# Performance work log

Measured on AMD Instinct MI355X. Metric: run time of the kernel, lower is better.

The kernel has to match this reference:

```python
import jax, jax.numpy as jnp
import numpy as np

N_NODES = 100000
N_EDGES = 1600000
D_IN = 128
D_OUT = 128
EPS = 1e-5


def setup_inputs() -> dict:
    key = jax.random.key(0)
    k1, k2, k3, k4, k5 = jax.random.split(key, 5)
    x = jax.random.normal(k1, (N_NODES, D_IN), dtype=jnp.float32)
    row = jax.random.randint(k2, (N_EDGES,), 0, N_NODES, dtype=jnp.int64)
    col = jax.random.randint(k3, (N_EDGES,), 0, N_NODES, dtype=jnp.int64)
    adj_vals = jax.random.uniform(k4, (N_EDGES,), dtype=jnp.float32)
    # Xavier-uniform init for weight, zeros for bias (as in the torch module)
    limit = float(np.sqrt(6.0 / (D_IN + D_OUT)))
    weight = jax.random.uniform(k5, (D_IN, D_OUT), minval=-limit, maxval=limit, dtype=jnp.float32)
    bias = jnp.zeros((D_OUT,), dtype=jnp.float32)
    return {"x": x, "row": row, "col": col, "adj_vals": adj_vals, "weight": weight, "bias": bias}


def reference(x, row, col, adj_vals, weight, bias):
    # degree = row-sum of sparse adj
    degree = jax.ops.segment_sum(adj_vals, row, num_segments=N_NODES)
    degree = jnp.where(degree == 0, EPS, degree)
    d_inv_sqrt = (degree + EPS) ** -0.5  # [N]
    # edge-wise symmetric normalization: D^-1/2 A D^-1/2
    edge_w = d_inv_sqrt[row] * adj_vals * d_inv_sqrt[col]  # [E]
    # SpMM: gather neighbor features, scale, scatter-add to destination rows
    msgs = edge_w[:, None] * x[col]  # [E, D_IN]
    agg = jax.ops.segment_sum(msgs, row, num_segments=N_NODES)  # [N, D_IN]
    return agg @ weight + bias
```

## Files before the change

kernel.cpp:

```cpp
#include <hip/hip_runtime.h>

#define NN 100000
#define NE 1600000
#define D  128
#define EPS 1e-5f

#define NBKT   782
#define NEB    391
#define EPB_H  4096
#define NSCAN  (NBKT*NEB)
#define CAP    2560
#define SLW    16

#define OFF_HCNT 0x0000000ULL
#define OFF_BTOT 0x0140000ULL
#define OFF_DINV 0x0150000ULL
#define OFF_RBC  0x0200000ULL
#define OFF_GREC 0x0280000ULL
#define OFF_ECOL 0x11C6000ULL
#define OFF_YB   0x1A00000ULL

typedef short short8 __attribute__((ext_vector_type(8)));
typedef float f32x4 __attribute__((ext_vector_type(4)));

static __device__ __forceinline__ unsigned f2bf(float f) {
    unsigned u = __float_as_uint(f);
    return (u + 0x7fffu + ((u >> 16) & 1u)) >> 16;
}

__global__ void k0h(const int* __restrict__ row, unsigned* __restrict__ hcnt) {
    __shared__ unsigned h[NBKT];
    int t = threadIdx.x, b = blockIdx.x;
    for (int i = t; i < NBKT; i += 256) h[i] = 0;
    __syncthreads();
    int ebeg = b * EPB_H;
    for (int i = t; i < EPB_H; i += 256) {
        int e = ebeg + i;
        if (e < NE) atomicAdd(&h[((unsigned)row[e]) >> 7], 1u);
    }
    __syncthreads();
    for (int i = t; i < NBKT; i += 256) hcnt[i * NEB + b] = h[i];
}

__global__ void k2s(unsigned* __restrict__ hcnt, unsigned* __restrict__ btot) {
    __shared__ unsigned s[256];
    int t = threadIdx.x, b = blockIdx.x;
    unsigned* hp = hcnt + (size_t)b * NEB;
    unsigned v0 = (2 * t     < NEB) ? hp[2 * t]     : 0;
    unsigned v1 = (2 * t + 1 < NEB) ? hp[2 * t + 1] : 0;
    unsigned sum = v0 + v1;
    s[t] = sum;
    __syncthreads();
    for (int d = 1; d < 256; d <<= 1) {
        unsigned u = (t >= d) ? s[t - d] : 0;
        __syncthreads();
        s[t] += u;
        __syncthreads();
    }
    unsigned base = s[t] - sum;
    if (2 * t     < NEB) hp[2 * t]     = base;
    if (2 * t + 1 < NEB) hp[2 * t + 1] = base + v0;
    if (t == 255) btot[b] = s[255];
}

__launch_bounds__(256)
__global__ void k3(const int* __restrict__ row, const int* __restrict__ col,
                   const float* __restrict__ adj, const unsigned* __restrict__ hcnt,
                   unsigned long long* __restrict__ grec) {
    __shared__ unsigned cur[NBKT];
    int t = threadIdx.x, b = blockIdx.x;
    for (int i = t; i < NBKT; i += 256)
        cur[i] = (unsigned)i * CAP + hcnt[i * NEB + b];
    __syncthreads();
    int ebeg = b * EPB_H;
    for (int i = t; i < EPB_H; i += 256) {
        int e = ebeg + i;
        if (e >= NE) continue;
        unsigned r = (unsigned)row[e];
        unsigned bkt = r >> 7;
        unsigned aq = (unsigned)rintf(adj[e] * 32767.0f);
        unsigned lo = (unsigned)col[e] | (aq << 17);
        unsigned dst = atomicAdd(&cur[bkt], 1u);
        if (dst < (bkt + 1) * (unsigned)CAP)
            grec[dst] = (unsigned long long)lo | ((unsigned long long)(r & 127u) << 32);
    }
}

__launch_bounds__(256, 2)
__global__ void k1g(const float* __restrict__ x, const float* __restrict__ w,
                    const unsigned* __restrict__ btot,
                    const unsigned long long* __restrict__ grec,
                    float* __restrict__ dinv_g, unsigned* __restrict__ rbcnt_g,
                    unsigned* __restrict__ ecol_g, unsigned short* __restrict__ yb) {
    __shared__ unsigned short sx[128 * 128];
    __shared__ unsigned short sw[128 * 128];
    __shared__ unsigned sdeg[128], scnt[128], srb[128], scur[128];
    __shared__ float sdv[128];
    unsigned* secol = (unsigned*)sx;
    int tid = threadIdx.x;
    int b = blockIdx.x;
    int base = b * 128;

    if (tid < 128) { sdeg[tid] = 0; scnt[tid] = 0; }
    __syncthreads();
    unsigned beg = (unsigned)b * CAP;
    unsigned n = min(btot[b], (unsigned)CAP);
    unsigned end = beg + n;
    for (unsigned p = beg + tid; p < end; p += 256) {
        unsigned long long rec = grec[p];
        unsigned rid = (unsigned)(rec >> 32) & 127u;
        atomicAdd(&sdeg[rid], ((unsigned)rec >> 17) & 0x7FFFu);
        atomicAdd(&scnt[rid], 1u);
    }
    __syncthreads();

    if (tid < 128) {
        float d = (float)sdeg[tid] * (1.0f / 32767.0f);
        d = (d == 0.0f) ? EPS : d;
        float dv = rsqrtf(d + EPS);
        sdv[tid] = dv;
        int r = base + tid;
        if (r < NN) dinv_g[r] = dv;
        srb[tid] = scnt[tid];
    }
    __syncthreads();
    for (int dd = 1; dd < 128; dd <<= 1) {
        unsigned u = (tid >= dd && tid < 128) ? srb[tid - dd] : 0;
        __syncthreads();
        if (tid < 128) srb[tid] += u;
        __syncthreads();
    }
    if (tid < 128) {
        unsigned rb = srb[tid] - scnt[tid];
        srb[tid] = rb;
        scur[tid] = rb;
        rbcnt_g[b * 128 + tid] = (rb << 16) | scnt[tid];
    }
    __syncthreads();

    for (unsigned p = beg + tid; p < end; p += 256) {
        unsigned long long rec = grec[p];
        unsigned rank = atomicAdd(&scur[(unsigned)(rec >> 32) & 127u], 1u);
        if (rank < CAP) secol[rank] = (unsigned)rec;
    }
    __syncthreads();
    for (unsigned i = tid; i < n; i += 256) ecol_g[(size_t)b * CAP + i] = secol[i];
    __syncthreads();

    #pragma unroll
    for (int i = 0; i < 8; ++i) {
        int task = i * 256 + tid;
        int nn = task & 127, ko = task >> 7;
        const float* wp = w + (size_t)(ko * 8) * D + nn;
        uint4 pk;
        pk.x = f2bf(wp[0])     | (f2bf(wp[D])     << 16);
        pk.y = f2bf(wp[2 * D]) | (f2bf(wp[3 * D]) << 16);
        pk.z = f2bf(wp[4 * D]) | (f2bf(wp[5 * D]) << 16);
        pk.w = f2bf(wp[6 * D]) | (f2bf(wp[7 * D]) << 16);
        int idx = (nn * 128 + ko * 8) ^ ((nn & 7) << 3);
        *(uint4*)(&sw[idx]) = pk;
    }
    #pragma unroll
    for (int i = 0; i < 8; ++i) {
        int task = i * 256 + tid;
        int ko = task & 15, r = task >> 4;
        int gr = base + r;
        float4 f0 = make_float4(0.f, 0.f, 0.f, 0.f), f1 = f0;
        if (gr < NN) {
            const float* xp = x + (size_t)gr * D + ko * 8;
            f0 = *(const float4*)xp;
            f1 = *(const float4*)(xp + 4);
        }
        uint4 pk;
        pk.x = f2bf(f0.x) | (f2bf(f0.y) << 16);
        pk.y = f2bf(f0.z) | (f2bf(f0.w) << 16);
        pk.z = f2bf(f1.x) | (f2bf(f1.y) << 16);
        pk.w = f2bf(f1.z) | (f2bf(f1.w) << 16);
        int idx = (r * 128 + ko * 8) ^ ((r & 7) << 3);
        *(uint4*)(&sx[idx]) = pk;
    }
    __syncthreads();

    int wv = tid >> 6, l = tid & 63;
    int lr = l & 15, g = l >> 4;

    f32x4 acc[2][8];
    #pragma unroll
    for (int ti = 0; ti < 2; ++ti)
        #pragma unroll
        for (int tj = 0; tj < 8; ++tj)
            acc[ti][tj] = (f32x4){0.f, 0.f, 0.f, 0.f};

    #pragma unroll
    for (int kc = 0; kc < 4; ++kc) {
        int kb = kc * 32 + g * 8;
        short8 a[2], bb[8];
        #pragma unroll
        for (int ti = 0; ti < 2; ++ti) {
            int r0 = wv * 32 + ti * 16 + lr;
            a[ti] = *(const short8*)(&sx[(r0 * 128 + kb) ^ ((r0 & 7) << 3)]);
        }
        #pragma unroll
        for (int tj = 0; tj < 8; ++tj) {
            int n0 = tj * 16 + lr;
            bb[tj] = *(const short8*)(&sw[(n0 * 128 + kb) ^ ((n0 & 7) << 3)]);
        }
        #pragma unroll
        for (int ti = 0; ti < 2; ++ti)
            #pragma unroll
            for (int tj = 0; tj < 8; ++tj)
                acc[ti][tj] = __builtin_amdgcn_mfma_f32_16x16x32_bf16(
                    a[ti], bb[tj], acc[ti][tj], 0, 0, 0);
    }

    #pragma unroll
    for (int ti = 0; ti < 2; ++ti) {
        #pragma unroll
        for (int reg = 0; reg < 4; ++reg) {
            int lrow = wv * 32 + ti * 16 + g * 4 + reg;
            int gr = base + lrow;
            if (gr < NN) {
                float dv = sdv[lrow];
                #pragma unroll
                for (int tj = 0; tj < 8; ++tj)
                    yb[(size_t)tj * ((size_t)NN * SLW) + (size_t)gr * SLW + lr] =
                        (unsigned short)f2bf(acc[ti][tj][reg] * dv);
            }
        }
    }
}

__launch_bounds__(256, 4)
__global__ void k4b(const unsigned* __restrict__ rbcnt_g, const unsigned* __restrict__ ecol_g,
                    const float* __restrict__ dinv, const unsigned short* __restrict__ ybs,
                    const float* __restrict__ bias, float* __restrict__ out) {
    __shared__ unsigned ecol[CAP + 8];
    __shared__ unsigned rb_l[128], cnt_l[128];
    __shared__ unsigned nsh;
    int t = threadIdx.x, bid = blockIdx.x;
    int s = bid & 7;
    int q = bid >> 3;
    const unsigned short* ys = ybs + (size_t)s * ((size_t)NN * SLW);

    if (t < 128) {
        unsigned v = rbcnt_g[q * 128 + t];
        rb_l[t] = v >> 16;
        cnt_l[t] = v & 0xFFFFu;
        if (t == 127) nsh = min((v >> 16) + (v & 0xFFFFu), (unsigned)CAP);
    }
    __syncthreads();
    unsigned n = nsh;
    const unsigned* eg = ecol_g + (size_t)q * CAP;
    for (unsigned i = t; i < n; i += 256) ecol[i] = eg[i];
    __syncthreads();

    int grp = t >> 1, lq = t & 1;
    int r = q * 128 + grp;
    if (r >= NN) return;
    unsigned jb = rb_l[grp];
    unsigned jend = min(jb + cnt_l[grp], (unsigned)CAP);

    float a0 = 0.f, a1 = 0.f, a2 = 0.f, a3 = 0.f;
    float a4 = 0.f, a5 = 0.f, a6 = 0.f, a7 = 0.f;

    for (unsigned j = jb; j < jend; j += 8) {
        unsigned ee[8];
        uint4 yq[8];
        float wv[8];
        int cm[8];
        unsigned c0 = ecol[j] & 0x1FFFFu;
        #pragma unroll
        for (int u = 0; u < 8; ++u) ee[u] = ecol[j + u];
        #pragma unroll
        for (int u = 0; u < 8; ++u)
            cm[u] = (j + u < jend) ? (int)(ee[u] & 0x1FFFFu) : (int)c0;
        #pragma unroll
        for (int u = 0; u < 8; ++u)
            yq[u] = *(const uint4*)(ys + (size_t)cm[u] * SLW + lq * 8);
        #pragma unroll
        for (int u = 0; u < 8; ++u)
            wv[u] = (j + u < jend) ? (float)(ee[u] >> 17) : 0.f;
        #pragma unroll
        for (int u = 0; u < 8; ++u) {
            a0 += wv[u] * __uint_as_float(yq[u].x << 16);
            a1 += wv[u] * __uint_as_float(yq[u].x & 0xffff0000u);
            a2 += wv[u] * __uint_as_float(yq[u].y << 16);
            a3 += wv[u] * __uint_as_float(yq[u].y & 0xffff0000u);
            a4 += wv[u] * __uint_as_float(yq[u].z << 16);
            a5 += wv[u] * __uint_as_float(yq[u].z & 0xffff0000u);
            a6 += wv[u] * __uint_as_float(yq[u].w << 16);
            a7 += wv[u] * __uint_as_float(yq[u].w & 0xffff0000u);
        }
    }

    float scale = dinv[r] * (1.0f / 32767.0f);
    const float4* bp = (const float4*)(bias + s * SLW + lq * 8);
    float4* op = (float4*)(out + (size_t)r * D + s * SLW + lq * 8);
    float4 b0 = bp[0], b1 = bp[1];
    op[0] = make_float4(a0 * scale + b0.x, a1 * scale + b0.y,
                        a2 * scale + b0.z, a3 * scale + b0.w);
    op[1] = make_float4(a4 * scale + b1.x, a5 * scale + b1.y,
                        a6 * scale + b1.z, a7 * scale + b1.w);
}

extern "C" void kernel_launch(void* const* d_in, const int* in_sizes, int n_in,
                              void* d_out, int out_size, void* d_ws, size_t ws_size,
                              hipStream_t stream) {
    const float* x    = (const float*)d_in[0];
    const int*   row  = (const int*)d_in[1];
    const int*   col  = (const int*)d_in[2];
    const float* adj  = (const float*)d_in[3];
    const float* wgt  = (const float*)d_in[4];
    const float* bias = (const float*)d_in[5];
    float* out = (float*)d_out;
    char*  ws  = (char*)d_ws;

    unsigned* hcnt  = (unsigned*)(ws + OFF_HCNT);
    unsigned* btot  = (unsigned*)(ws + OFF_BTOT);
    float*    dinv  = (float*)(ws + OFF_DINV);
    unsigned* rbcnt = (unsigned*)(ws + OFF_RBC);
    unsigned long long* grec = (unsigned long long*)(ws + OFF_GREC);
    unsigned* ecolg = (unsigned*)(ws + OFF_ECOL);
    unsigned short* yb = (unsigned short*)(ws + OFF_YB);

    k0h<<<NEB, 256, 0, stream>>>(row, hcnt);
    k2s<<<NBKT, 256, 0, stream>>>(hcnt, btot);
    k3 <<<NEB, 256, 0, stream>>>(row, col, adj, hcnt, grec);
    k1g<<<NBKT, 256, 0, stream>>>(x, wgt, btot, grec, dinv, rbcnt, ecolg, yb);
    k4b<<<NBKT * 8, 256, 0, stream>>>(rbcnt, ecolg, dinv, yb, bias, out);
}
```

Baseline: 148.1 us.

## Store projected features row-major and split SpMM into two 64-column halves

```diff
diff --git a/kernel.cpp b/kernel.cpp
--- a/kernel.cpp
+++ b/kernel.cpp
@@ -10,7 +10,6 @@
 #define EPB_H  4096
 #define NSCAN  (NBKT*NEB)
 #define CAP    2560
-#define SLW    16
 
 #define OFF_HCNT 0x0000000ULL
 #define OFF_BTOT 0x0140000ULL
@@ -223,24 +222,26 @@
                 float dv = sdv[lrow];
                 #pragma unroll
                 for (int tj = 0; tj < 8; ++tj)
-                    yb[(size_t)tj * ((size_t)NN * SLW) + (size_t)gr * SLW + lr] =
+                    yb[(size_t)gr * D + tj * 16 + lr] =
                         (unsigned short)f2bf(acc[ti][tj][reg] * dv);
             }
         }
     }
 }
 
-__launch_bounds__(256, 4)
+__launch_bounds__(512, 4)
 __global__ void k4b(const unsigned* __restrict__ rbcnt_g, const unsigned* __restrict__ ecol_g,
-                    const float* __restrict__ dinv, const unsigned short* __restrict__ ybs,
+                    const float* __restrict__ dinv, const unsigned short* __restrict__ yb,
                     const float* __restrict__ bias, float* __restrict__ out) {
     __shared__ unsigned ecol[CAP + 8];
     __shared__ unsigned rb_l[128], cnt_l[128];
     __shared__ unsigned nsh;
     int t = threadIdx.x, bid = blockIdx.x;
-    int s = bid & 7;
-    int q = bid >> 3;
-    const unsigned short* ys = ybs + (size_t)s * ((size_t)NN * SLW);
+    int xcd = bid & 7;
+    int ch  = xcd >> 2;
+    int q   = (bid >> 3) * 4 + (xcd & 3);
+    if (q >= NBKT) return;
+    int cb = ch * 64;
 
     if (t < 128) {
         unsigned v = rbcnt_g[q * 128 + t];
@@ -251,56 +252,60 @@
     __syncthreads();
     unsigned n = nsh;
     const unsigned* eg = ecol_g + (size_t)q * CAP;
-    for (unsigned i = t; i < n; i += 256) ecol[i] = eg[i];
-    __syncthreads();
-
-    int grp = t >> 1, lq = t & 1;
-    int r = q * 128 + grp;
-    if (r >= NN) return;
-    unsigned jb = rb_l[grp];
-    unsigned jend = min(jb + cnt_l[grp], (unsigned)CAP);
-
-    float a0 = 0.f, a1 = 0.f, a2 = 0.f, a3 = 0.f;
-    float a4 = 0.f, a5 = 0.f, a6 = 0.f, a7 = 0.f;
-
-    for (unsigned j = jb; j < jend; j += 8) {
-        unsigned ee[8];
-        uint4 yq[8];
-        float wv[8];
-        int cm[8];
-        unsigned c0 = ecol[j] & 0x1FFFFu;
-        #pragma unroll
-        for (int u = 0; u < 8; ++u) ee[u] = ecol[j + u];
-        #pragma unroll
-        for (int u = 0; u < 8; ++u)
-            cm[u] = (j + u < jend) ? (int)(ee[u] & 0x1FFFFu) : (int)c0;
-        #pragma unroll
-        for (int u = 0; u < 8; ++u)
-            yq[u] = *(const uint4*)(ys + (size_t)cm[u] * SLW + lq * 8);
-        #pragma unroll
-        for (int u = 0; u < 8; ++u)
-            wv[u] = (j + u < jend) ? (float)(ee[u] >> 17) : 0.f;
-        #pragma unroll
-        for (int u = 0; u < 8; ++u) {
-            a0 += wv[u] * __uint_as_float(yq[u].x << 16);
-            a1 += wv[u] * __uint_as_float(yq[u].x & 0xffff0000u);
-            a2 += wv[u] * __uint_as_float(yq[u].y << 16);
-            a3 += wv[u] * __uint_as_float(yq[u].y & 0xffff0000u);
-            a4 += wv[u] * __uint_as_float(yq[u].z << 16);
-            a5 += wv[u] * __uint_as_float(yq[u].z & 0xffff0000u);
-            a6 += wv[u] * __uint_as_float(yq[u].w << 16);
-            a7 += wv[u] * __uint_as_float(yq[u].w & 0xffff0000u);
-        }
-    }
-
-    float scale = dinv[r] * (1.0f / 32767.0f);
-    const float4* bp = (const float4*)(bias + s * SLW + lq * 8);
-    float4* op = (float4*)(out + (size_t)r * D + s * SLW + lq * 8);
-    float4 b0 = bp[0], b1 = bp[1];
-    op[0] = make_float4(a0 * scale + b0.x, a1 * scale + b0.y,
-                        a2 * scale + b0.z, a3 * scale + b0.w);
-    op[1] = make_float4(a4 * scale + b1.x, a5 * scale + b1.y,
-                        a6 * scale + b1.z, a7 * scale + b1.w);
+    for (unsigned i = t; i < n; i += 512) ecol[i] = eg[i];
+    __syncthreads();
+
+    int grp = t >> 3, lq = t & 7;
+    #pragma unroll
+    for (int k = 0; k < 2; ++k) {
+        int rowlo = (k << 6) + grp;
+        int r = q * 128 + rowlo;
+        if (r >= NN) continue;
+        unsigned jb = rb_l[rowlo];
+        unsigned jend = min(jb + cnt_l[rowlo], (unsigned)CAP);
+
+        float a0 = 0.f, a1 = 0.f, a2 = 0.f, a3 = 0.f;
+        float a4 = 0.f, a5 = 0.f, a6 = 0.f, a7 = 0.f;
+
+        for (unsigned j = jb; j < jend; j += 8) {
+            unsigned ee[8];
+            uint4 yq[8];
+            float wv[8];
+            int cm[8];
+            unsigned c0 = ecol[j] & 0x1FFFFu;
+            #pragma unroll
+            for (int u = 0; u < 8; ++u) ee[u] = ecol[j + u];
+            #pragma unroll
+            for (int u = 0; u < 8; ++u)
+                cm[u] = (j + u < jend) ? (int)(ee[u] & 0x1FFFFu) : (int)c0;
+            #pragma unroll
+            for (int u = 0; u < 8; ++u)
+                yq[u] = *(const uint4*)(yb + (size_t)cm[u] * D + cb + lq * 8);
+            #pragma unroll
+            for (int u = 0; u < 8; ++u)
+                wv[u] = (j + u < jend) ? (float)(ee[u] >> 17) : 0.f;
+            #pragma unroll
+            for (int u = 0; u < 8; ++u) {
+                a0 += wv[u] * __uint_as_float(yq[u].x << 16);
+                a1 += wv[u] * __uint_as_float(yq[u].x & 0xffff0000u);
+                a2 += wv[u] * __uint_as_float(yq[u].y << 16);
+                a3 += wv[u] * __uint_as_float(yq[u].y & 0xffff0000u);
+                a4 += wv[u] * __uint_as_float(yq[u].z << 16);
+                a5 += wv[u] * __uint_as_float(yq[u].z & 0xffff0000u);
+                a6 += wv[u] * __uint_as_float(yq[u].w << 16);
+                a7 += wv[u] * __uint_as_float(yq[u].w & 0xffff0000u);
+            }
+        }
+
+        float scale = dinv[r] * (1.0f / 32767.0f);
+        const float4* bp = (const float4*)(bias + cb + lq * 8);
+        float4* op = (float4*)(out + (size_t)r * D + cb + lq * 8);
+        float4 b0 = bp[0], b1 = bp[1];
+        op[0] = make_float4(a0 * scale + b0.x, a1 * scale + b0.y,
+                            a2 * scale + b0.z, a3 * scale + b0.w);
+        op[1] = make_float4(a4 * scale + b1.x, a5 * scale + b1.y,
+                            a6 * scale + b1.z, a7 * scale + b1.w);
+    }
 }
 
 extern "C" void kernel_launch(void* const* d_in, const int* in_sizes, int n_in,
@@ -327,5 +332,5 @@
     k2s<<<NBKT, 256, 0, stream>>>(hcnt, btot);
     k3 <<<NEB, 256, 0, stream>>>(row, col, adj, hcnt, grec);
     k1g<<<NBKT, 256, 0, stream>>>(x, wgt, btot, grec, dinv, rbcnt, ecolg, yb);
-    k4b<<<NBKT * 8, 256, 0, stream>>>(rbcnt, ecolg, dinv, yb, bias, out);
-}
+    k4b<<<1568, 512, 0, stream>>>(rbcnt, ecolg, dinv, yb, bias, out);
+}
```

Measured after the change: 126.6 us (median of 2 runs). 1.17x faster.
